# Performance work log

Hardware: AMD Instinct MI355X
Metric: run time of the kernel (lower is better)

The kernel has to match this reference:

```python
import jax, jax.numpy as jnp
import numpy as np

B, T, C = 2, 2048, 1024
H = 16
D = C // H  # head_size = 64
FF = 4 * C
EPS = 1e-5


def _layernorm(x, g, b):
    mu = jnp.mean(x, axis=-1, keepdims=True)
    var = jnp.var(x, axis=-1, keepdims=True)
    return (x - mu) * jax.lax.rsqrt(var + EPS) * g + b


def setup_inputs() -> dict:
    key = jax.random.key(0)
    ks = jax.random.split(key, 12)
    s_in = 1.0 / np.sqrt(C)
    s_ff = 1.0 / np.sqrt(FF)
    return {
        "x": jax.random.normal(ks[0], (B, T, C), jnp.float32),
        "Wq": jax.random.uniform(ks[1], (H, C, D), jnp.float32, -s_in, s_in),
        "Wk": jax.random.uniform(ks[2], (H, C, D), jnp.float32, -s_in, s_in),
        "Wv": jax.random.uniform(ks[3], (H, C, D), jnp.float32, -s_in, s_in),
        "Wo": jax.random.uniform(ks[4], (C, C), jnp.float32, -s_in, s_in),
        "bo": jax.random.uniform(ks[5], (C,), jnp.float32, -s_in, s_in),
        "W1": jax.random.uniform(ks[6], (C, FF), jnp.float32, -s_in, s_in),
        "b1": jax.random.uniform(ks[7], (FF,), jnp.float32, -s_in, s_in),
        "W2": jax.random.uniform(ks[8], (FF, C), jnp.float32, -s_ff, s_ff),
        "b2": jax.random.uniform(ks[9], (C,), jnp.float32, -s_ff, s_ff),
        "g1": jnp.ones((C,), jnp.float32),
        "be1": jnp.zeros((C,), jnp.float32),
        "g2": jnp.ones((C,), jnp.float32),
        "be2": jnp.zeros((C,), jnp.float32),
    }


def reference(x, Wq, Wk, Wv, Wo, bo, W1, b1, W2, b2, g1, be1, g2, be2):
    h = _layernorm(x, g1, be1)
    # per-head projections (no bias), vectorized over heads
    q = jnp.einsum("btc,hcd->bhtd", h, Wq)
    k = jnp.einsum("btc,hcd->bhtd", h, Wk)
    v = jnp.einsum("btc,hcd->bhtd", h, Wv)
    # NOTE: original scales by n_embd**-0.5 (C, not head_size) -- faithful
    scores = jnp.einsum("bhtd,bhsd->bhts", q, k) * (C ** -0.5)
    causal = jnp.tril(jnp.ones((T, T), bool))
    scores = jnp.where(causal, scores, -jnp.inf)
    att = jax.nn.softmax(scores, axis=-1)
    out = jnp.einsum("bhts,bhsd->bhtd", att, v)
    out = out.transpose(0, 2, 1, 3).reshape(B, T, C)  # concat heads
    x = out @ Wo + bo + x  # attn residual (dropout=0 -> identity)
    h2 = _layernorm(x, g2, be2)
    ff = jax.nn.relu(h2 @ W1 + b1) @ W2 + b2
    return x + ff
```

## Files before the change

kernel.cpp:

```cpp
#include <hip/hip_runtime.h>
#include <stdint.h>

typedef unsigned short ushort_t;
typedef __attribute__((ext_vector_type(8))) short bf16x8;
typedef __attribute__((ext_vector_type(4))) float f32x4;

__device__ __forceinline__ unsigned short f2b(float f) {
  unsigned u = __float_as_uint(f);
  u += 0x7fffu + ((u >> 16) & 1u);
  return (unsigned short)(u >> 16);
}

__device__ __forceinline__ void async16(const void* g, void* l) {
  __builtin_amdgcn_global_load_lds(
      (const __attribute__((address_space(1))) void*)g,
      (__attribute__((address_space(3))) void*)l, 16, 0, 0);
}

__global__ __launch_bounds__(256) void ln_kernel(
    const float* __restrict__ x, const float* __restrict__ g,
    const float* __restrict__ be, ushort_t* __restrict__ out) {
  const int C = 1024;
  int row = blockIdx.x;
  const float4* xr = (const float4*)(x + (size_t)row * C);
  int tid = threadIdx.x;
  float4 v = xr[tid];
  float s = v.x + v.y + v.z + v.w;
  float sq = v.x * v.x + v.y * v.y + v.z * v.z + v.w * v.w;
  #pragma unroll
  for (int off = 32; off > 0; off >>= 1) {
    s += __shfl_xor(s, off);
    sq += __shfl_xor(sq, off);
  }
  __shared__ float ss[4], ssq[4];
  int wv = tid >> 6;
  if ((tid & 63) == 0) { ss[wv] = s; ssq[wv] = sq; }
  __syncthreads();
  s = ss[0] + ss[1] + ss[2] + ss[3];
  sq = ssq[0] + ssq[1] + ssq[2] + ssq[3];
  float mu = s * (1.f / C);
  float var = sq * (1.f / C) - mu * mu;
  float rs = rsqrtf(var + 1e-5f);
  float4 gv = ((const float4*)g)[tid];
  float4 bv = ((const float4*)be)[tid];
  ushort4 o;
  o.x = f2b((v.x - mu) * rs * gv.x + bv.x);
  o.y = f2b((v.y - mu) * rs * gv.y + bv.y);
  o.z = f2b((v.z - mu) * rs * gv.z + bv.z);
  o.w = f2b((v.w - mu) * rs * gv.w + bv.w);
  ((ushort4*)(out + (size_t)row * C))[tid] = o;
}

__global__ __launch_bounds__(256) void transpose_cast_kernel(
    const float* __restrict__ in, ushort_t* __restrict__ out, int R, int Cin) {
  __shared__ float tile[32][33];
  int bz = blockIdx.z;
  in += (size_t)bz * R * Cin;
  out += (size_t)bz * R * Cin;
  int c0 = blockIdx.x * 32, r0 = blockIdx.y * 32;
  int tx = threadIdx.x, ty = threadIdx.y;
  #pragma unroll
  for (int i = 0; i < 4; i++)
    tile[ty + 8 * i][tx] = in[(size_t)(r0 + ty + 8 * i) * Cin + c0 + tx];
  __syncthreads();
  #pragma unroll
  for (int i = 0; i < 4; i++)
    out[(size_t)(c0 + ty + 8 * i) * R + r0 + tx] = f2b(tile[tx][ty + 8 * i]);
}

__global__ __launch_bounds__(256) void transpose_v_kernel(
    const ushort_t* __restrict__ qkv, ushort_t* __restrict__ vt) {
  __shared__ ushort_t tile[32][33];
  int bh = blockIdx.z;
  int b = bh >> 4, h = bh & 15;
  int d0 = blockIdx.x * 32, t0 = blockIdx.y * 32;
  int tx = threadIdx.x, ty = threadIdx.y;
  #pragma unroll
  for (int i = 0; i < 4; i++)
    tile[ty + 8 * i][tx] =
        qkv[(size_t)(b * 2048 + t0 + ty + 8 * i) * 3072 + 2048 + h * 64 + d0 + tx];
  __syncthreads();
  #pragma unroll
  for (int i = 0; i < 4; i++)
    vt[(size_t)(bh * 64 + d0 + ty + 8 * i) * 2048 + t0 + tx] = tile[tx][ty + 8 * i];
}

template <int MT, int N, int K, int FLAGS>
__global__ __launch_bounds__(256, 2) void gemm_bt_kernel(
    const ushort_t* __restrict__ A, const ushort_t* __restrict__ Bt,
    const float* __restrict__ bias, const float* __restrict__ resid,
    void* __restrict__ outv) {
  constexpr int MI = MT / 32;
  __shared__ ushort_t Als[2][MT * 32];
  __shared__ ushort_t Bls[2][128 * 32];
  int tid = threadIdx.x, w = tid >> 6, lane = tid & 63, quad = lane >> 4, l16 = lane & 15;
  int bn0 = blockIdx.x * 128, bm0 = blockIdx.y * MT;
  int wm = (w >> 1) * (MT / 2), wn = (w & 1) * 64;
  f32x4 acc[MI][4];
  #pragma unroll
  for (int i = 0; i < MI; i++)
    #pragma unroll
    for (int j = 0; j < 4; j++) acc[i][j] = f32x4{0.f, 0.f, 0.f, 0.f};
  const ushort_t* Ag = A + (size_t)bm0 * K;
  const ushort_t* Bg = Bt + (size_t)bn0 * K;
  int lr = lane >> 2, lco = (lane & 3) * 8;
  auto stage = [&](int k0, int bi) {
    if constexpr (MT == 128) {
      async16(Ag + (size_t)(w * 32 + lr) * K + k0 + lco, &Als[bi][w * 1024]);
      async16(Ag + (size_t)(w * 32 + 16 + lr) * K + k0 + lco, &Als[bi][w * 1024 + 512]);
    } else {
      async16(Ag + (size_t)(w * 16 + lr) * K + k0 + lco, &Als[bi][w * 512]);
    }
    async16(Bg + (size_t)(w * 32 + lr) * K + k0 + lco, &Bls[bi][w * 1024]);
    async16(Bg + (size_t)(w * 32 + 16 + lr) * K + k0 + lco, &Bls[bi][w * 1024 + 512]);
  };
  stage(0, 0);
  int s = 0;
  for (int k0 = 0; k0 < K; k0 += 32, s ^= 1) {
    __syncthreads();
    if (k0 + 32 < K) stage(k0 + 32, s ^ 1);
    bf16x8 af[MI], bf[4];
    #pragma unroll
    for (int i = 0; i < MI; i++)
      af[i] = *(const bf16x8*)&Als[s][(wm + i * 16 + l16) * 32 + quad * 8];
    #pragma unroll
    for (int j = 0; j < 4; j++)
      bf[j] = *(const bf16x8*)&Bls[s][(wn + j * 16 + l16) * 32 + quad * 8];
    #pragma unroll
    for (int i = 0; i < MI; i++)
      #pragma unroll
      for (int j = 0; j < 4; j++)
        acc[i][j] = __builtin_amdgcn_mfma_f32_16x16x32_bf16(af[i], bf[j], acc[i][j], 0, 0, 0);
  }
  #pragma unroll
  for (int i = 0; i < MI; i++)
    #pragma unroll
    for (int j = 0; j < 4; j++)
      #pragma unroll
      for (int r = 0; r < 4; r++) {
        int row = bm0 + wm + i * 16 + quad * 4 + r;
        int col = bn0 + wn + j * 16 + l16;
        float v = acc[i][j][r];
        if constexpr (FLAGS & 4) v += bias[col];
        if constexpr (FLAGS & 8) v += resid[(size_t)row * N + col];
        if constexpr (FLAGS & 1) v = fmaxf(v, 0.f);
        if constexpr ((FLAGS & 2) != 0)
          ((ushort_t*)outv)[(size_t)row * N + col] = f2b(v);
        else
          ((float*)outv)[(size_t)row * N + col] = v;
      }
}

__global__ __launch_bounds__(256, 4) void attn_kernel(
    const ushort_t* __restrict__ qkv, const ushort_t* __restrict__ vt,
    ushort_t* __restrict__ out) {
  const int T = 2048, CC = 3072;
  __shared__ ushort_t Kls[2][2 * 64 * 32];
  __shared__ ushort_t Vls[2][2 * 64 * 32];
  int fid = blockIdx.x;
  int bh = (fid & 7) * 4 + ((fid >> 3) & 3);
  int qb = 31 - (fid >> 5);
  int b = bh >> 4, h = bh & 15;
  int q0 = qb * 64;
  int tid = threadIdx.x, w = tid >> 6, lane = tid & 63, quad = lane >> 4, l16 = lane & 15;
  int srow = w * 16 + (lane >> 2);
  int sco = (lane & 3) * 8;
  const ushort_t* kg = qkv + (size_t)(b * T + srow) * CC + 1024 + h * 64 + sco;
  const ushort_t* vg = vt + (size_t)(bh * 64 + srow) * T + sco;
  int q0s = q0 + w * 16;
  int trow = q0s + l16;
  const ushort_t* qp = qkv + (size_t)(b * T + trow) * CC + h * 64 + quad * 8;
  bf16x8 aq[2] = { *(const bf16x8*)qp, *(const bf16x8*)(qp + 32) };
  f32x4 O[4];
  #pragma unroll
  for (int i = 0; i < 4; i++) O[i] = f32x4{0.f, 0.f, 0.f, 0.f};
  float mrun = -1e30f, lrun = 0.f;
  const float ksc = 0.03125f * 1.44269504f;
  int src0 = (quad & 1) * 32 + l16;
  int src1 = src0 + 16;
  bool hiq = quad >= 2;
  auto stage = [&](int kb, int bi) {
    int s0 = kb * 64;
    async16(kg + (size_t)s0 * CC, &Kls[bi][w * 512]);
    async16(kg + (size_t)s0 * CC + 32, &Kls[bi][2048 + w * 512]);
    async16(vg + s0, &Vls[bi][w * 512]);
    async16(vg + s0 + 32, &Vls[bi][2048 + w * 512]);
  };
  stage(0, 0);
  for (int kb = 0; kb <= qb; kb++) {
    __syncthreads();
    if (kb < qb) stage(kb + 1, (kb + 1) & 1);
    int bi = kb & 1;
    int s0 = kb * 64;
    bf16x8 kfr[4][2], vfr[4][2];
    #pragma unroll
    for (int t = 0; t < 4; t++)
      #pragma unroll
      for (int ks = 0; ks < 2; ks++) {
        kfr[t][ks] = *(const bf16x8*)&Kls[bi][(ks * 64 + t * 16 + l16) * 32 + quad * 8];
        vfr[t][ks] = *(const bf16x8*)&Vls[bi][(ks * 64 + t * 16 + l16) * 32 + quad * 8];
      }
    f32x4 st[4];
    #pragma unroll
    for (int t = 0; t < 4; t++) {
      st[t] = f32x4{0.f, 0.f, 0.f, 0.f};
      #pragma unroll
      for (int ks = 0; ks < 2; ks++)
        st[t] = __builtin_amdgcn_mfma_f32_16x16x32_bf16(kfr[t][ks], aq[ks], st[t], 0, 0, 0);
    }
    float sv[4][4];
    float vmax = -1e30f;
    if (kb == qb) {
      #pragma unroll
      for (int t = 0; t < 4; t++)
        #pragma unroll
        for (int r = 0; r < 4; r++) {
          float sc = st[t][r] * ksc;
          int scol = s0 + t * 16 + quad * 4 + r;
          if (scol > trow) sc = -1e30f;
          sv[t][r] = sc;
          vmax = fmaxf(vmax, sc);
        }
    } else {
      #pragma unroll
      for (int t = 0; t < 4; t++)
        #pragma unroll
        for (int r = 0; r < 4; r++) {
          float sc = st[t][r] * ksc;
          sv[t][r] = sc;
          vmax = fmaxf(vmax, sc);
        }
    }
    vmax = fmaxf(vmax, __shfl_xor(vmax, 16));
    vmax = fmaxf(vmax, __shfl_xor(vmax, 32));
    float mnew = fmaxf(mrun, vmax);
    float alpha = __builtin_amdgcn_exp2f(mrun - mnew);
    mrun = mnew;
    float psum = 0.f;
    int pk[4][2];
    #pragma unroll
    for (int t = 0; t < 4; t++) {
      float p0 = __builtin_amdgcn_exp2f(sv[t][0] - mnew);
      float p1 = __builtin_amdgcn_exp2f(sv[t][1] - mnew);
      float p2 = __builtin_amdgcn_exp2f(sv[t][2] - mnew);
      float p3 = __builtin_amdgcn_exp2f(sv[t][3] - mnew);
      psum += (p0 + p1) + (p2 + p3);
      pk[t][0] = (int)((unsigned)f2b(p0) | ((unsigned)f2b(p1) << 16));
      pk[t][1] = (int)((unsigned)f2b(p2) | ((unsigned)f2b(p3) << 16));
    }
    psum += __shfl_xor(psum, 16);
    psum += __shfl_xor(psum, 32);
    lrun = lrun * alpha + psum;
    #pragma unroll
    for (int dt = 0; dt < 4; dt++) O[dt] *= alpha;
    #pragma unroll
    for (int g32 = 0; g32 < 2; g32++) {
      int t0 = 2 * g32, t1 = t0 + 1;
      int a0 = __shfl(pk[t0][0], src0), b0 = __shfl(pk[t1][0], src0);
      int a1 = __shfl(pk[t0][1], src0), b1 = __shfl(pk[t1][1], src0);
      int a2 = __shfl(pk[t0][0], src1), b2 = __shfl(pk[t1][0], src1);
      int a3 = __shfl(pk[t0][1], src1), b3 = __shfl(pk[t1][1], src1);
      union { int4 i; bf16x8 h; } u;
      u.i.x = hiq ? b0 : a0;
      u.i.y = hiq ? b1 : a1;
      u.i.z = hiq ? b2 : a2;
      u.i.w = hiq ? b3 : a3;
      #pragma unroll
      for (int dt = 0; dt < 4; dt++)
        O[dt] = __builtin_amdgcn_mfma_f32_16x16x32_bf16(vfr[dt][g32], u.h, O[dt], 0, 0, 0);
    }
  }
  float inv = 1.f / lrun;
  #pragma unroll
  for (int dt = 0; dt < 4; dt++) {
    ushort4 o;
    unsigned short* op = (unsigned short*)&o;
    #pragma unroll
    for (int r = 0; r < 4; r++) op[r] = f2b(O[dt][r] * inv);
    *(ushort4*)&out[(size_t)(b * T + trow) * 1024 + h * 64 + dt * 16 + quad * 4] = o;
  }
}

extern "C" void kernel_launch(void* const* d_in, const int* in_sizes, int n_in,
                              void* d_out, int out_size, void* d_ws, size_t ws_size,
                              hipStream_t stream) {
  const int B = 2, T = 2048, C = 1024, H = 16, D = 64, FF = 4096;
  const int M = B * T;
  const float* x   = (const float*)d_in[0];
  const float* Wq  = (const float*)d_in[1];
  const float* Wk  = (const float*)d_in[2];
  const float* Wv  = (const float*)d_in[3];
  const float* Wo  = (const float*)d_in[4];
  const float* bo  = (const float*)d_in[5];
  const float* W1  = (const float*)d_in[6];
  const float* b1  = (const float*)d_in[7];
  const float* W2  = (const float*)d_in[8];
  const float* b2  = (const float*)d_in[9];
  const float* g1  = (const float*)d_in[10];
  const float* be1 = (const float*)d_in[11];
  const float* g2  = (const float*)d_in[12];
  const float* be2 = (const float*)d_in[13];
  float* out = (float*)d_out;

  char* ws = (char*)d_ws;
  size_t off = 0;
  auto alloc = [&](size_t bytes) {
    void* p = ws + off;
    off += (bytes + 255) & ~(size_t)255;
    return p;
  };
  ushort_t* qkvt = (ushort_t*)alloc((size_t)3 * C * C * 2);
  ushort_t* wot  = (ushort_t*)alloc((size_t)C * C * 2);
  ushort_t* w1t  = (ushort_t*)alloc((size_t)FF * C * 2);
  ushort_t* w2t  = (ushort_t*)alloc((size_t)C * FF * 2);
  ushort_t* hbuf = (ushort_t*)alloc((size_t)M * C * 2);
  ushort_t* big  = (ushort_t*)alloc((size_t)M * FF * 2);
  ushort_t* vtb  = (ushort_t*)alloc((size_t)M * C * 2);
  ushort_t* aout = (ushort_t*)alloc((size_t)M * C * 2);
  float*    x2   = (float*)alloc((size_t)M * C * 4);

  dim3 tb(32, 8);
  transpose_cast_kernel<<<dim3(D / 32, C / 32, H), tb, 0, stream>>>(Wq, qkvt, C, D);
  transpose_cast_kernel<<<dim3(D / 32, C / 32, H), tb, 0, stream>>>(Wk, qkvt + (size_t)C * C, C, D);
  transpose_cast_kernel<<<dim3(D / 32, C / 32, H), tb, 0, stream>>>(Wv, qkvt + (size_t)2 * C * C, C, D);
  transpose_cast_kernel<<<dim3(C / 32, C / 32, 1), tb, 0, stream>>>(Wo, wot, C, C);
  transpose_cast_kernel<<<dim3(FF / 32, C / 32, 1), tb, 0, stream>>>(W1, w1t, C, FF);
  transpose_cast_kernel<<<dim3(C / 32, FF / 32, 1), tb, 0, stream>>>(W2, w2t, FF, C);
  ln_kernel<<<M, 256, 0, stream>>>(x, g1, be1, hbuf);
  gemm_bt_kernel<128, 3072, 1024, 2><<<dim3(24, 32), 256, 0, stream>>>(
      hbuf, qkvt, nullptr, nullptr, big);
  transpose_v_kernel<<<dim3(2, T / 32, B * H), tb, 0, stream>>>(big, vtb);
  attn_kernel<<<1024, 256, 0, stream>>>(big, vtb, aout);
  gemm_bt_kernel<64, 1024, 1024, 4 | 8><<<dim3(8, 64), 256, 0, stream>>>(
      aout, wot, bo, x, x2);
  ln_kernel<<<M, 256, 0, stream>>>(x2, g2, be2, hbuf);
  gemm_bt_kernel<128, 4096, 1024, 1 | 2 | 4><<<dim3(32, 32), 256, 0, stream>>>(
      hbuf, w1t, b1, nullptr, big);
  gemm_bt_kernel<64, 1024, 4096, 4 | 8><<<dim3(8, 64), 256, 0, stream>>>(
      big, w2t, b2, x2, out);
}
```

Baseline: 386.5 us.

## Split-K the FFN down-projection into two halves with a separate reduce kernel

The FFN second GEMM (K=4096) now uses 128x128 tiles with a two-way split-K over blockIdx.z. Each half writes fp32 partials into reused workspace buffers, and a new reduce kernel adds the partials, bias and residual. The 64-row tile variant is dropped, so the Wo projection also moves to 128x128 tiles, which halves its grid to 256 blocks. The intent is more data reuse per tile while split-K keeps enough blocks in flight for the long-K GEMM, at the cost of extra fp32 partial traffic and one more launch.

```diff
diff --git a/kernel.cpp b/kernel.cpp
--- a/kernel.cpp
+++ b/kernel.cpp
@@ -51,6 +51,23 @@
   ((ushort4*)(out + (size_t)row * C))[tid] = o;
 }
 
+__global__ __launch_bounds__(256) void reduce2_kernel(
+    const float* __restrict__ p0, const float* __restrict__ p1,
+    const float* __restrict__ bias, const float* __restrict__ resid,
+    float* __restrict__ out) {
+  int idx = blockIdx.x * 256 + threadIdx.x;
+  float4 a = ((const float4*)p0)[idx];
+  float4 b = ((const float4*)p1)[idx];
+  float4 r = ((const float4*)resid)[idx];
+  float4 bi = ((const float4*)bias)[idx & 255];
+  float4 o;
+  o.x = a.x + b.x + r.x + bi.x;
+  o.y = a.y + b.y + r.y + bi.y;
+  o.z = a.z + b.z + r.z + bi.z;
+  o.w = a.w + b.w + r.w + bi.w;
+  ((float4*)out)[idx] = o;
+}
+
 __global__ __launch_bounds__(256) void transpose_cast_kernel(
     const float* __restrict__ in, ushort_t* __restrict__ out, int R, int Cin) {
   __shared__ float tile[32][33];
@@ -85,55 +102,54 @@
     vt[(size_t)(bh * 64 + d0 + ty + 8 * i) * 2048 + t0 + tx] = tile[tx][ty + 8 * i];
 }
 
-template <int MT, int N, int K, int FLAGS>
+template <int N, int K, int FLAGS, int SK>
 __global__ __launch_bounds__(256, 2) void gemm_bt_kernel(
     const ushort_t* __restrict__ A, const ushort_t* __restrict__ Bt,
     const float* __restrict__ bias, const float* __restrict__ resid,
-    void* __restrict__ outv) {
-  constexpr int MI = MT / 32;
-  __shared__ ushort_t Als[2][MT * 32];
+    void* __restrict__ outv, float* __restrict__ pp0, float* __restrict__ pp1) {
+  constexpr int KS = K / SK;
+  __shared__ ushort_t Als[2][128 * 32];
   __shared__ ushort_t Bls[2][128 * 32];
   int tid = threadIdx.x, w = tid >> 6, lane = tid & 63, quad = lane >> 4, l16 = lane & 15;
-  int bn0 = blockIdx.x * 128, bm0 = blockIdx.y * MT;
-  int wm = (w >> 1) * (MT / 2), wn = (w & 1) * 64;
-  f32x4 acc[MI][4];
-  #pragma unroll
-  for (int i = 0; i < MI; i++)
+  int bn0 = blockIdx.x * 128, bm0 = blockIdx.y * 128;
+  int koff = (SK > 1) ? blockIdx.z * KS : 0;
+  int wm = (w >> 1) * 64, wn = (w & 1) * 64;
+  f32x4 acc[4][4];
+  #pragma unroll
+  for (int i = 0; i < 4; i++)
     #pragma unroll
     for (int j = 0; j < 4; j++) acc[i][j] = f32x4{0.f, 0.f, 0.f, 0.f};
-  const ushort_t* Ag = A + (size_t)bm0 * K;
-  const ushort_t* Bg = Bt + (size_t)bn0 * K;
+  const ushort_t* Ag = A + (size_t)bm0 * K + koff;
+  const ushort_t* Bg = Bt + (size_t)bn0 * K + koff;
   int lr = lane >> 2, lco = (lane & 3) * 8;
   auto stage = [&](int k0, int bi) {
-    if constexpr (MT == 128) {
-      async16(Ag + (size_t)(w * 32 + lr) * K + k0 + lco, &Als[bi][w * 1024]);
-      async16(Ag + (size_t)(w * 32 + 16 + lr) * K + k0 + lco, &Als[bi][w * 1024 + 512]);
-    } else {
-      async16(Ag + (size_t)(w * 16 + lr) * K + k0 + lco, &Als[bi][w * 512]);
-    }
+    async16(Ag + (size_t)(w * 32 + lr) * K + k0 + lco, &Als[bi][w * 1024]);
+    async16(Ag + (size_t)(w * 32 + 16 + lr) * K + k0 + lco, &Als[bi][w * 1024 + 512]);
     async16(Bg + (size_t)(w * 32 + lr) * K + k0 + lco, &Bls[bi][w * 1024]);
     async16(Bg + (size_t)(w * 32 + 16 + lr) * K + k0 + lco, &Bls[bi][w * 1024 + 512]);
   };
   stage(0, 0);
   int s = 0;
-  for (int k0 = 0; k0 < K; k0 += 32, s ^= 1) {
+  for (int k0 = 0; k0 < KS; k0 += 32, s ^= 1) {
     __syncthreads();
-    if (k0 + 32 < K) stage(k0 + 32, s ^ 1);
-    bf16x8 af[MI], bf[4];
-    #pragma unroll
-    for (int i = 0; i < MI; i++)
+    if (k0 + 32 < KS) stage(k0 + 32, s ^ 1);
+    bf16x8 af[4], bf[4];
+    #pragma unroll
+    for (int i = 0; i < 4; i++)
       af[i] = *(const bf16x8*)&Als[s][(wm + i * 16 + l16) * 32 + quad * 8];
     #pragma unroll
     for (int j = 0; j < 4; j++)
       bf[j] = *(const bf16x8*)&Bls[s][(wn + j * 16 + l16) * 32 + quad * 8];
     #pragma unroll
-    for (int i = 0; i < MI; i++)
+    for (int i = 0; i < 4; i++)
       #pragma unroll
       for (int j = 0; j < 4; j++)
         acc[i][j] = __builtin_amdgcn_mfma_f32_16x16x32_bf16(af[i], bf[j], acc[i][j], 0, 0, 0);
   }
-  #pragma unroll
-  for (int i = 0; i < MI; i++)
+  float* pdst = nullptr;
+  if constexpr (SK > 1) pdst = blockIdx.z ? pp1 : pp0;
+  #pragma unroll
+  for (int i = 0; i < 4; i++)
     #pragma unroll
     for (int j = 0; j < 4; j++)
       #pragma unroll
@@ -141,13 +157,17 @@
         int row = bm0 + wm + i * 16 + quad * 4 + r;
         int col = bn0 + wn + j * 16 + l16;
         float v = acc[i][j][r];
-        if constexpr (FLAGS & 4) v += bias[col];
-        if constexpr (FLAGS & 8) v += resid[(size_t)row * N + col];
-        if constexpr (FLAGS & 1) v = fmaxf(v, 0.f);
-        if constexpr ((FLAGS & 2) != 0)
-          ((ushort_t*)outv)[(size_t)row * N + col] = f2b(v);
-        else
-          ((float*)outv)[(size_t)row * N + col] = v;
+        if constexpr (SK > 1) {
+          pdst[(size_t)row * N + col] = v;
+        } else {
+          if constexpr (FLAGS & 4) v += bias[col];
+          if constexpr (FLAGS & 8) v += resid[(size_t)row * N + col];
+          if constexpr (FLAGS & 1) v = fmaxf(v, 0.f);
+          if constexpr ((FLAGS & 2) != 0)
+            ((ushort_t*)outv)[(size_t)row * N + col] = f2b(v);
+          else
+            ((float*)outv)[(size_t)row * N + col] = v;
+        }
       }
 }
 
@@ -318,6 +338,8 @@
   ushort_t* vtb  = (ushort_t*)alloc((size_t)M * C * 2);
   ushort_t* aout = (ushort_t*)alloc((size_t)M * C * 2);
   float*    x2   = (float*)alloc((size_t)M * C * 4);
+  float* pf0 = (float*)vtb;
+  float* pf1 = (float*)qkvt;
 
   dim3 tb(32, 8);
   transpose_cast_kernel<<<dim3(D / 32, C / 32, H), tb, 0, stream>>>(Wq, qkvt, C, D);
@@ -327,15 +349,16 @@
   transpose_cast_kernel<<<dim3(FF / 32, C / 32, 1), tb, 0, stream>>>(W1, w1t, C, FF);
   transpose_cast_kernel<<<dim3(C / 32, FF / 32, 1), tb, 0, stream>>>(W2, w2t, FF, C);
   ln_kernel<<<M, 256, 0, stream>>>(x, g1, be1, hbuf);
-  gemm_bt_kernel<128, 3072, 1024, 2><<<dim3(24, 32), 256, 0, stream>>>(
-      hbuf, qkvt, nullptr, nullptr, big);
+  gemm_bt_kernel<3072, 1024, 2, 1><<<dim3(24, 32), 256, 0, stream>>>(
+      hbuf, qkvt, nullptr, nullptr, big, nullptr, nullptr);
   transpose_v_kernel<<<dim3(2, T / 32, B * H), tb, 0, stream>>>(big, vtb);
   attn_kernel<<<1024, 256, 0, stream>>>(big, vtb, aout);
-  gemm_bt_kernel<64, 1024, 1024, 4 | 8><<<dim3(8, 64), 256, 0, stream>>>(
-      aout, wot, bo, x, x2);
+  gemm_bt_kernel<1024, 1024, 4 | 8, 1><<<dim3(8, 32), 256, 0, stream>>>(
+      aout, wot, bo, x, x2, nullptr, nullptr);
   ln_kernel<<<M, 256, 0, stream>>>(x2, g2, be2, hbuf);
-  gemm_bt_kernel<128, 4096, 1024, 1 | 2 | 4><<<dim3(32, 32), 256, 0, stream>>>(
-      hbuf, w1t, b1, nullptr, big);
-  gemm_bt_kernel<64, 1024, 4096, 4 | 8><<<dim3(8, 64), 256, 0, stream>>>(
-      big, w2t, b2, x2, out);
-}
+  gemm_bt_kernel<4096, 1024, 1 | 2 | 4, 1><<<dim3(32, 32), 256, 0, stream>>>(
+      hbuf, w1t, b1, nullptr, big, nullptr, nullptr);
+  gemm_bt_kernel<1024, 4096, 0, 2><<<dim3(8, 32, 2), 256, 0, stream>>>(
+      big, w2t, nullptr, nullptr, nullptr, pf0, pf1);
+  reduce2_kernel<<<M * C / 1024, 256, 0, stream>>>(pf0, pf1, b2, x2, out);
+}
```

Result: no change. 380.9 us (-1.4%).
